# Kernel tuning notes

Hardware: AMD Instinct MI355X
Metric: run time of the kernel (lower is better)

Reference implementation:

```python
import jax, jax.numpy as jnp
import numpy as np

E = 16   # num_experts
K = 4    # num_activated_experts
B, S, H, I = 4, 1024, 1024, 2048


def setup_inputs() -> dict:
    key = jax.random.key(0)
    k0, k1, k2, k3 = jax.random.split(key, 4)
    scale = 0.02
    return {
        "hidden_states": jax.random.normal(k0, (B, S, H), jnp.float32),
        "router_w": jax.random.normal(k1, (H, E), jnp.float32) * scale,
        "router_b": jnp.zeros((E,), jnp.float32),
        "w1": jax.random.normal(k2, (E, H, I), jnp.float32) * scale,
        "b1": jnp.zeros((E, I), jnp.float32),
        "w2": jax.random.normal(k3, (E, I, H), jnp.float32) * scale,
        "b2": jnp.zeros((E, H), jnp.float32),
    }


def reference(hidden_states, router_w, router_b, w1, b1, w2, b2):
    b, s, h = hidden_states.shape
    # router: softmax over experts, pick top-k, renormalize top-k weights
    logits = hidden_states @ router_w + router_b            # [B,S,E]
    probs = jax.nn.softmax(logits, axis=-1)
    topw, topi = jax.lax.top_k(probs, K)                    # [B,S,K]
    topw = topw / jnp.sum(topw, axis=-1, keepdims=True)
    # scatter top-k weights into dense per-expert combine weights [B,S,E]
    combine = jnp.sum(
        jax.nn.one_hot(topi, E, dtype=hidden_states.dtype) * topw[..., None],
        axis=2,
    )
    x = hidden_states.reshape(b * s, h)                     # [T,H]
    c = combine.reshape(b * s, E)                           # [T,E]

    def body(acc, expert):
        w1e, b1e, w2e, b2e, ce = expert
        hmid = jax.nn.gelu(x @ w1e + b1e, approximate=False)  # [T,I]
        return acc + (hmid @ w2e + b2e) * ce[:, None], None

    out, _ = jax.lax.scan(body, jnp.zeros_like(x), (w1, b1, w2, b2, c.T))
    return out.reshape(b, s, h)
```

## Files before the change

### kernel.cpp

```cpp
#include <hip/hip_runtime.h>

#define T_TOK 4096
#define H_DIM 1024
#define I_DIM 2048
#define E_NUM 16
#define K_TOP 4
#define BM 128
#define BK 32
#define MAX_TILES 144
#define PAD_PAIRS (MAX_TILES * BM)
#define RW_Q 4104

typedef __attribute__((ext_vector_type(8))) short s16x8;
typedef __attribute__((ext_vector_type(4))) float f32x4;
typedef __attribute__((ext_vector_type(4))) unsigned short u16x4;
typedef __attribute__((ext_vector_type(8))) unsigned short u16x8;

#define DSR(dst, addr, off) \
  asm volatile("ds_read_b128 %0, %1 offset:" #off : "=v"(dst) : "v"(addr))

__device__ __forceinline__ unsigned short f2bf(float f) {
  unsigned u = __float_as_uint(f);
  u += 0x7fffu + ((u >> 16) & 1u);
  return (unsigned short)(u >> 16);
}

__device__ __forceinline__ void mfma_bf16(const s16x8& a, const s16x8& b, f32x4& c) {
  asm("v_mfma_f32_16x16x32_bf16 %0, %1, %2, %0" : "+v"(c) : "v"(a), "v"(b));
}

__device__ __forceinline__ void gld16(const void* g, void* l) {
  __builtin_amdgcn_global_load_lds(
      (const __attribute__((address_space(1))) unsigned int*)g,
      (__attribute__((address_space(3))) unsigned int*)l, 16, 0, 0);
}

__device__ __forceinline__ int tile_map(const int* counts, int ty, int* tsp) {
  int e = -1, acc = 0, base = 0;
#pragma unroll
  for (int ee = 0; ee < E_NUM; ++ee) {
    int tc = (counts[ee] + 127) >> 7;
    if (ty >= acc && ty < acc + tc) {
      e = ee;
      *tsp = base + ((ty - acc) << 7);
    }
    acc += tc;
    base += tc << 7;
  }
  return e;
}

__global__ __launch_bounds__(256) void router_kernel(
    const float* __restrict__ x, const float* __restrict__ rw,
    const float* __restrict__ rb, int* __restrict__ topi,
    float* __restrict__ topw, int* __restrict__ counts,
    unsigned short* __restrict__ xb) {
  __shared__ float rws[4 * RW_Q];
  const int tid = threadIdx.x;
  {
    const size_t base = (size_t)blockIdx.x * 16 * H_DIM;
#pragma unroll
    for (int it = 0; it < 8; ++it) {
      size_t idx = base + ((size_t)(it * 256 + tid)) * 8;
      f32x4 a = *(const f32x4*)(x + idx);
      f32x4 b = *(const f32x4*)(x + idx + 4);
      u16x8 o;
      o[0] = f2bf(a[0]); o[1] = f2bf(a[1]); o[2] = f2bf(a[2]); o[3] = f2bf(a[3]);
      o[4] = f2bf(b[0]); o[5] = f2bf(b[1]); o[6] = f2bf(b[2]); o[7] = f2bf(b[3]);
      *(u16x8*)(xb + idx) = o;
    }
  }
  for (int idx = tid * 4; idx < H_DIM * E_NUM; idx += 256 * 4) {
    f32x4 v = *(const f32x4*)(rw + idx);
    int h = idx >> 4, e0 = idx & 15;
    *(f32x4*)&rws[(h >> 8) * RW_Q + (h & 255) * 16 + e0] = v;
  }
  __syncthreads();
  const int w = tid >> 6, l = tid & 63;
  const int e = l & 15, q = l >> 4;
  const float rbe = rb[e];
  const float* ldsb = &rws[q * RW_Q + e];
#pragma unroll
  for (int i = 0; i < 4; ++i) {
    const int t = blockIdx.x * 16 + w * 4 + i;
    const float* xr = x + (size_t)t * H_DIM + (q << 8);
    float acc = 0.f;
#pragma unroll 8
    for (int hh = 0; hh < 256; hh += 4) {
      f32x4 xv = *(const f32x4*)(xr + hh);
      acc += xv[0] * ldsb[(hh + 0) * 16];
      acc += xv[1] * ldsb[(hh + 1) * 16];
      acc += xv[2] * ldsb[(hh + 2) * 16];
      acc += xv[3] * ldsb[(hh + 3) * 16];
    }
    acc += __shfl_xor(acc, 16);
    acc += __shfl_xor(acc, 32);
    float logit = acc + rbe;
    float m = logit;
    m = fmaxf(m, __shfl_xor(m, 1));
    m = fmaxf(m, __shfl_xor(m, 2));
    m = fmaxf(m, __shfl_xor(m, 4));
    m = fmaxf(m, __shfl_xor(m, 8));
    float ex = expf(logit - m);
    int rank = 0;
    const int b16 = l & 48;
#pragma unroll
    for (int j = 0; j < 16; ++j) {
      float vj = __shfl(ex, b16 + j);
      rank += (vj > ex) || (vj == ex && j < e);
    }
    float sel = (rank < K_TOP) ? ex : 0.f;
    float subs = sel;
    subs += __shfl_xor(subs, 1);
    subs += __shfl_xor(subs, 2);
    subs += __shfl_xor(subs, 4);
    subs += __shfl_xor(subs, 8);
    if (q == 0 && rank < K_TOP) {
      topi[t * K_TOP + rank] = e;
      topw[t * K_TOP + rank] = ex / subs;
      atomicAdd(&counts[e], 1);
    }
  }
}

__global__ __launch_bounds__(256) void scatter_kernel(
    const int* __restrict__ topi, const float* __restrict__ topw,
    const int* __restrict__ counts, int* __restrict__ cursor,
    int* __restrict__ pairTok, float* __restrict__ pairW,
    int* __restrict__ pairPos) {
  int padBase[E_NUM];
  int base = 0;
#pragma unroll
  for (int ee = 0; ee < E_NUM; ++ee) {
    padBase[ee] = base;
    base += ((counts[ee] + 127) >> 7) << 7;
  }
  const int t = blockIdx.x * 256 + threadIdx.x;
#pragma unroll
  for (int k = 0; k < K_TOP; ++k) {
    int e = topi[t * K_TOP + k];
    int pos = atomicAdd(&cursor[e], 1);
    int idx = padBase[e] + pos;
    pairTok[idx] = t;
    pairW[idx] = topw[t * K_TOP + k];
    pairPos[t * K_TOP + k] = idx;
  }
#pragma unroll
  for (int ee = 0; ee < E_NUM; ++ee) {
    int c = counts[ee];
    int padded = ((c + 127) >> 7) << 7;
    int o = c + t;
    if (o < padded) pairTok[padBase[ee] + o] = -1;
  }
}

__device__ __forceinline__ void transpose_tile(const float* __restrict__ src,
                                               unsigned short* __restrict__ dst,
                                               int R, int C, int tx, int ty) {
  int r0 = ty * 64, c0 = tx * 64;
  __shared__ float tle[64][65];
  int rr = threadIdx.x >> 4, cc = (threadIdx.x & 15) * 4;
#pragma unroll
  for (int i = 0; i < 4; ++i) {
    f32x4 v = *(const f32x4*)(src + (size_t)(r0 + rr + 16 * i) * C + c0 + cc);
    tle[rr + 16 * i][cc + 0] = v[0];
    tle[rr + 16 * i][cc + 1] = v[1];
    tle[rr + 16 * i][cc + 2] = v[2];
    tle[rr + 16 * i][cc + 3] = v[3];
  }
  __syncthreads();
#pragma unroll
  for (int i = 0; i < 4; ++i) {
    int oc = c0 + rr + 16 * i;
    u16x4 o;
    o[0] = f2bf(tle[cc + 0][rr + 16 * i]);
    o[1] = f2bf(tle[cc + 1][rr + 16 * i]);
    o[2] = f2bf(tle[cc + 2][rr + 16 * i]);
    o[3] = f2bf(tle[cc + 3][rr + 16 * i]);
    *(u16x4*)(dst + (size_t)oc * R + r0 + cc) = o;
  }
}

__global__ __launch_bounds__(256) void transpose_kernel(
    const float* __restrict__ src, unsigned short* __restrict__ dst, int R,
    int C) {
  size_t es = (size_t)R * C;
  transpose_tile(src + es * blockIdx.z, dst + es * blockIdx.z, R, C,
                 blockIdx.x, blockIdx.y);
}

__global__ __launch_bounds__(256) void transpose2_kernel(
    const float* __restrict__ w1, const float* __restrict__ w2,
    unsigned short* __restrict__ wT1, unsigned short* __restrict__ wT2) {
  const int bid = blockIdx.x;
  const size_t es = (size_t)H_DIM * I_DIM;
  if (bid < 8192) {
    const int e = bid >> 9, tb = bid & 511;
    transpose_tile(w1 + es * e, wT1 + es * e, H_DIM, I_DIM, tb & 31, tb >> 5);
  } else {
    const int eb = bid - 8192;
    const int e = eb >> 9, tb = eb & 511;
    transpose_tile(w2 + es * e, wT2 + es * e, I_DIM, H_DIM, tb & 15, tb >> 4);
  }
}

__global__ __launch_bounds__(256, 4) void gemm1_kernel(
    const unsigned short* __restrict__ xb, const unsigned short* __restrict__ w1t,
    const float* __restrict__ b1, unsigned short* __restrict__ hmid,
    const int* __restrict__ pairTok, const int* __restrict__ counts) {
  const int bid = blockIdx.x;
  const int lin = (bid & 7) * 288 + (bid >> 3);
  const int tx = lin & 15, ty = lin >> 4;
  int tsp = 0;
  const int e = tile_map(counts, ty, &tsp);
  if (e < 0) return;
  const int n0 = tx * 128;
  __shared__ unsigned short As[2][BM * BK];
  __shared__ unsigned short Bs[2][BM * BK];
  const int tid = threadIdx.x, w = tid >> 6, l = tid & 63;
  const int rbase = w * 16 + (l >> 2);
  const int segp = (l & 3) ^ ((l >> 3) & 3);
  int tok0 = pairTok[tsp + rbase];
  if (tok0 < 0) tok0 = 0;
  int tok1 = pairTok[tsp + rbase + 64];
  if (tok1 < 0) tok1 = 0;
  const char* gA0 = (const char*)(xb + (size_t)tok0 * H_DIM) + segp * 16;
  const char* gA1 = (const char*)(xb + (size_t)tok1 * H_DIM) + segp * 16;
  const unsigned short* wbase = w1t + (size_t)e * I_DIM * H_DIM;
  const char* gB0 = (const char*)(wbase + (size_t)(n0 + rbase) * H_DIM) + segp * 16;
  const char* gB1 = (const char*)(wbase + (size_t)(n0 + rbase + 64) * H_DIM) + segp * 16;

  f32x4 acc[4][4];
#pragma unroll
  for (int m = 0; m < 4; ++m)
#pragma unroll
    for (int n = 0; n < 4; ++n) acc[m][n] = f32x4{0.f, 0.f, 0.f, 0.f};

  const int wr = w >> 1, wc = w & 1, lrow = l & 15, g = l >> 4;
  const int gs = g ^ ((l >> 1) & 3);
  const int NK = H_DIM / BK;

  gld16(gA0, &As[0][w * 512]);
  gld16(gA1, &As[0][2048 + w * 512]);
  gld16(gB0, &Bs[0][w * 512]);
  gld16(gB1, &Bs[0][2048 + w * 512]);

  for (int kt = 0; kt < NK; ++kt) {
    __syncthreads();
    if (kt + 1 < NK) {
      const int kb = (kt + 1) * 64;
      const int nb = (kt + 1) & 1;
      gld16(gA0 + kb, &As[nb][w * 512]);
      gld16(gA1 + kb, &As[nb][2048 + w * 512]);
      gld16(gB0 + kb, &Bs[nb][w * 512]);
      gld16(gB1 + kb, &Bs[nb][2048 + w * 512]);
    }
    const int cb = kt & 1;
    const s16x8* Ap = (const s16x8*)As[cb];
    const s16x8* Bp = (const s16x8*)Bs[cb];
    s16x8 av[4], bv[4];
#pragma unroll
    for (int m = 0; m < 4; ++m) av[m] = Ap[(wr * 64 + m * 16 + lrow) * 4 + gs];
#pragma unroll
    for (int n = 0; n < 4; ++n) bv[n] = Bp[(wc * 64 + n * 16 + lrow) * 4 + gs];
#pragma unroll
    for (int m = 0; m < 4; ++m)
#pragma unroll
      for (int n = 0; n < 4; ++n) mfma_bf16(av[m], bv[n], acc[m][n]);
  }

  const float* b1e = b1 + (size_t)e * I_DIM;
#pragma unroll
  for (int m = 0; m < 4; ++m) {
    const int rw0 = wr * 64 + m * 16 + g * 4;
#pragma unroll
    for (int n = 0; n < 4; ++n) {
      const int col = n0 + wc * 64 + n * 16 + lrow;
      const float bb = b1e[col];
      f32x4 v = acc[m][n];
#pragma unroll
      for (int j = 0; j < 4; ++j) {
        const int p = tsp + rw0 + j;
        float xv = v[j] + bb;
        float y = 0.7978845608028654f * (xv + 0.044715f * xv * xv * xv);
        float ey = __expf(2.f * y);
        float th = 1.f - 2.f / (ey + 1.f);
        float ge = 0.5f * xv * (1.f + th);
        hmid[(size_t)p * I_DIM + col] = f2bf(ge);
      }
    }
  }
}

__global__ __launch_bounds__(256, 3) void gemm2_kernel(
    const unsigned short* __restrict__ hmid,
    const unsigned short* __restrict__ w2t, const float* __restrict__ b2,
    float* __restrict__ out, unsigned short* __restrict__ poA,
    unsigned short* __restrict__ poB, const int* __restrict__ pairTok,
    const float* __restrict__ pairW, const int* __restrict__ counts, int mode) {
  __shared__ char LDS[49152];
  const int bid = blockIdx.x;
  const int nchunk = (mode == 2) ? 288 : 144;
  const int lin = (bid & 7) * nchunk + (bid >> 3);
  const int kh = (mode == 2) ? (lin & 1) : 0;
  const int tx = (mode == 2) ? ((lin >> 1) & 7) : (lin & 7);
  const int ty = (mode == 2) ? (lin >> 4) : (lin >> 3);
  int tsp = 0;
  const int e = tile_map(counts, ty, &tsp);
  if (e < 0) return;
  const int n0 = tx * 128;
  const int tid = threadIdx.x, w = tid >> 6, l = tid & 63;
  const int rbase = w * 16 + (l >> 2);
  const int segp = (l & 3) ^ ((l >> 3) & 3);
  const size_t koff = (size_t)kh * 2048;
  const char* gA0 =
      (const char*)(hmid + (size_t)(tsp + rbase) * I_DIM) + segp * 16 + koff;
  const char* gA1 =
      (const char*)(hmid + (size_t)(tsp + rbase + 64) * I_DIM) + segp * 16 + koff;
  const unsigned short* wbase = w2t + (size_t)e * H_DIM * I_DIM;
  const char* gB0 =
      (const char*)(wbase + (size_t)(n0 + rbase) * I_DIM) + segp * 16 + koff;
  const char* gB1 =
      (const char*)(wbase + (size_t)(n0 + rbase + 64) * I_DIM) + segp * 16 + koff;

  f32x4 acc[4][4];
#pragma unroll
  for (int m = 0; m < 4; ++m)
#pragma unroll
    for (int n = 0; n < 4; ++n) acc[m][n] = f32x4{0.f, 0.f, 0.f, 0.f};

  const int wr = w >> 1, wc = w & 1, lrow = l & 15, g = l >> 4;
  const int gs = g ^ ((l >> 1) & 3);
  const int NK = (mode == 2) ? 32 : 64;

  char* dA = LDS + w * 1024;
  char* dB = LDS + 24576 + w * 1024;
  const unsigned ldsb = (unsigned)(uintptr_t)&LDS[0];
  const unsigned aRd = ldsb + (unsigned)((wr * 64 + lrow) * 64 + gs * 16);
  const unsigned bRd = ldsb + 24576u + (unsigned)((wc * 64 + lrow) * 64 + gs * 16);

  asm volatile("s_waitcnt vmcnt(0)" ::: "memory");
  gld16(gA0, dA);        gld16(gA1, dA + 4096);
  gld16(gB0, dB);        gld16(gB1, dB + 4096);
  gld16(gA0 + 64, dA + 8192);  gld16(gA1 + 64, dA + 8192 + 4096);
  gld16(gB0 + 64, dB + 8192);  gld16(gB1 + 64, dB + 8192 + 4096);

  int srd = 0, sst = 2;
  for (int t = 0; t < NK; ++t) {
    if (t + 1 < NK)
      asm volatile("s_waitcnt vmcnt(4)" ::: "memory");
    else
      asm volatile("s_waitcnt vmcnt(0)" ::: "memory");
    asm volatile("s_barrier" ::: "memory");
    const int tau = t + 2;
    if (tau < NK) {
      const size_t kb = (size_t)tau * 64;
      char* da = dA + sst * 8192;
      char* db = dB + sst * 8192;
      gld16(gA0 + kb, da);  gld16(gA1 + kb, da + 4096);
      gld16(gB0 + kb, db);  gld16(gB1 + kb, db + 4096);
    }
    const unsigned so = (unsigned)(srd * 8192);
    const unsigned aS = aRd + so, bS = bRd + so;
    s16x8 av[4], bv[4];
    DSR(bv[0], bS, 0);    DSR(bv[1], bS, 1024);
    DSR(bv[2], bS, 2048); DSR(bv[3], bS, 3072);
    DSR(av[0], aS, 0);    DSR(av[1], aS, 1024);
    DSR(av[2], aS, 2048); DSR(av[3], aS, 3072);
    asm volatile("s_waitcnt lgkmcnt(0)" ::: "memory");
    __builtin_amdgcn_sched_barrier(0);
    __builtin_amdgcn_s_setprio(1);
#pragma unroll
    for (int m = 0; m < 4; ++m)
#pragma unroll
      for (int n = 0; n < 4; ++n) mfma_bf16(av[m], bv[n], acc[m][n]);
    __builtin_amdgcn_s_setprio(0);
    srd = (srd == 2) ? 0 : srd + 1;
    sst = (sst == 2) ? 0 : sst + 1;
  }
  __builtin_amdgcn_sched_barrier(0);

  if (mode >= 1) {
    unsigned short* po = (kh == 0) ? poA : poB;
#pragma unroll
    for (int m = 0; m < 4; ++m) {
      const int rw0 = wr * 64 + m * 16 + g * 4;
#pragma unroll
      for (int n = 0; n < 4; ++n) {
        const int col = n0 + wc * 64 + n * 16 + lrow;
        f32x4 v = acc[m][n];
#pragma unroll
        for (int j = 0; j < 4; ++j)
          po[(size_t)(tsp + rw0 + j) * H_DIM + col] = f2bf(v[j]);
      }
    }
  } else {
    const float* b2e = b2 + (size_t)e * H_DIM;
#pragma unroll
    for (int m = 0; m < 4; ++m) {
      const int rw0 = wr * 64 + m * 16 + g * 4;
#pragma unroll
      for (int j = 0; j < 4; ++j) {
        const int p = tsp + rw0 + j;
        const int tok = pairTok[p];
        if (tok < 0) continue;
        const float pw = pairW[p];
        float* orow = out + (size_t)tok * H_DIM;
#pragma unroll
        for (int n = 0; n < 4; ++n) {
          const int col = n0 + wc * 64 + n * 16 + lrow;
          float val = (acc[m][n][j] + b2e[col]) * pw;
          atomicAdd(orow + col, val);
        }
      }
    }
  }
}

__global__ __launch_bounds__(256) void combine_kernel(
    const unsigned short* __restrict__ poA, const unsigned short* __restrict__ poB,
    const int* __restrict__ pairPos, const int* __restrict__ topi,
    const float* __restrict__ topw, const float* __restrict__ b2,
    float* __restrict__ out, int nbuf) {
  const int t = blockIdx.x * 2 + (threadIdx.x >> 7);
  const int c0 = (threadIdx.x & 127) * 8;
  float o[8];
#pragma unroll
  for (int j = 0; j < 8; ++j) o[j] = 0.f;
#pragma unroll
  for (int k = 0; k < K_TOP; ++k) {
    const int e = topi[t * K_TOP + k];
    const float pw = topw[t * K_TOP + k];
    const int pos = pairPos[t * K_TOP + k];
    u16x8 va = *(const u16x8*)(poA + (size_t)pos * H_DIM + c0);
    u16x8 vb;
    if (nbuf == 2) vb = *(const u16x8*)(poB + (size_t)pos * H_DIM + c0);
    const float* b2r = b2 + (size_t)e * H_DIM + c0;
#pragma unroll
    for (int j = 0; j < 8; ++j) {
      float hv = __uint_as_float((unsigned)va[j] << 16);
      if (nbuf == 2) hv += __uint_as_float((unsigned)vb[j] << 16);
      o[j] += pw * (hv + b2r[j]);
    }
  }
  float* orow = out + (size_t)t * H_DIM + c0;
  *(f32x4*)orow = f32x4{o[0], o[1], o[2], o[3]};
  *(f32x4*)(orow + 4) = f32x4{o[4], o[5], o[6], o[7]};
}

extern "C" void kernel_launch(void* const* d_in, const int* in_sizes, int n_in,
                              void* d_out, int out_size, void* d_ws,
                              size_t ws_size, hipStream_t stream) {
  const float* x = (const float*)d_in[0];
  const float* rw = (const float*)d_in[1];
  const float* rb = (const float*)d_in[2];
  const float* w1 = (const float*)d_in[3];
  const float* b1 = (const float*)d_in[4];
  const float* w2 = (const float*)d_in[5];
  const float* b2 = (const float*)d_in[6];
  float* out = (float*)d_out;
  char* ws = (char*)d_ws;

  const size_t xbSz = (size_t)T_TOK * H_DIM * 2;
  const size_t poSz = (size_t)PAD_PAIRS * H_DIM * 2;
  const size_t wtSz = (size_t)E_NUM * H_DIM * I_DIM * 2;
  const size_t hmSz = (size_t)PAD_PAIRS * I_DIM * 2;
  const size_t smallSz = (size_t)T_TOK * K_TOP * 4 * 3
                         + (size_t)PAD_PAIRS * 4 * 2 + 128;
  const size_t need3 = poSz * 2 + wtSz * 2 + hmSz + smallSz;
  const size_t need2 = poSz * 2 + wtSz + hmSz + smallSz;
  const size_t need1 = poSz + wtSz + hmSz + smallSz;
  const size_t need0 = xbSz + wtSz + hmSz + smallSz;
  int mode;
  if (ws_size >= need3) mode = 3;
  else if (ws_size >= need2) mode = 2;
  else if (ws_size >= need1) mode = 1;
  else if (ws_size >= need0) mode = 0;
  else return;

  size_t off = 0;
  unsigned short* xb = (unsigned short*)(ws + off);
  unsigned short* poA = (unsigned short*)(ws + off);
  off += (mode >= 1) ? poSz : xbSz;
  unsigned short* poB = (unsigned short*)(ws + off);
  if (mode >= 2) off += poSz;
  unsigned short* wT1 = (unsigned short*)(ws + off);
  off += wtSz;
  unsigned short* wT2 = wT1;
  if (mode == 3) { wT2 = (unsigned short*)(ws + off); off += wtSz; }
  unsigned short* hmid = (unsigned short*)(ws + off);
  off += hmSz;
  int* topi = (int*)(ws + off);      off += (size_t)T_TOK * K_TOP * 4;
  float* topw = (float*)(ws + off);  off += (size_t)T_TOK * K_TOP * 4;
  int* pairPos = (int*)(ws + off);   off += (size_t)T_TOK * K_TOP * 4;
  int* pairTok = (int*)(ws + off);   off += (size_t)PAD_PAIRS * 4;
  float* pairW = (float*)(ws + off); off += (size_t)PAD_PAIRS * 4;
  int* counts = (int*)(ws + off);    off += 64;
  int* cursor = (int*)(ws + off);    off += 64;

  const int gmode = (mode >= 2) ? 2 : mode;

  hipMemsetAsync(counts, 0, 128, stream);
  if (gmode == 0) hipMemsetAsync(out, 0, (size_t)T_TOK * H_DIM * 4, stream);

  router_kernel<<<T_TOK / 16, 256, 0, stream>>>(x, rw, rb, topi, topw, counts,
                                                xb);
  scatter_kernel<<<T_TOK / 256, 256, 0, stream>>>(topi, topw, counts, cursor,
                                                  pairTok, pairW, pairPos);
  if (mode == 3) {
    transpose2_kernel<<<16384, 256, 0, stream>>>(w1, w2, wT1, wT2);
    gemm1_kernel<<<16 * MAX_TILES, 256, 0, stream>>>(xb, wT1, b1, hmid, pairTok,
                                                     counts);
  } else {
    transpose_kernel<<<dim3(I_DIM / 64, H_DIM / 64, E_NUM), 256, 0, stream>>>(
        w1, wT1, H_DIM, I_DIM);
    gemm1_kernel<<<16 * MAX_TILES, 256, 0, stream>>>(xb, wT1, b1, hmid, pairTok,
                                                     counts);
    transpose_kernel<<<dim3(H_DIM / 64, I_DIM / 64, E_NUM), 256, 0, stream>>>(
        w2, wT2, I_DIM, H_DIM);
  }
  gemm2_kernel<<<(gmode == 2 ? 16 : 8) * MAX_TILES, 256, 0, stream>>>(
      hmid, wT2, b2, out, poA, poB, pairTok, pairW, counts, gmode);
  if (gmode >= 1)
    combine_kernel<<<T_TOK / 2, 256, 0, stream>>>(poA, poB, pairPos, topi, topw,
                                                  b2, out, gmode);
}
```

Measured before the change: 412.5 us.

## Fuse router with w1 transpose and overlap w2 transpose with gemm1

```diff
diff --git a/kernel.cpp b/kernel.cpp
--- a/kernel.cpp
+++ b/kernel.cpp
@@ -9,7 +9,6 @@
 #define BK 32
 #define MAX_TILES 144
 #define PAD_PAIRS (MAX_TILES * BM)
-#define RW_Q 4104
 
 typedef __attribute__((ext_vector_type(8))) short s16x8;
 typedef __attribute__((ext_vector_type(4))) float f32x4;
@@ -50,15 +49,41 @@
   return e;
 }
 
-__global__ __launch_bounds__(256) void router_kernel(
-    const float* __restrict__ x, const float* __restrict__ rw,
+__device__ __forceinline__ void transpose_tile(const float* __restrict__ src,
+                                               unsigned short* __restrict__ dst,
+                                               int R, int C, int tx, int ty) {
+  int r0 = ty * 64, c0 = tx * 64;
+  __shared__ float tle[64][65];
+  int rr = threadIdx.x >> 4, cc = (threadIdx.x & 15) * 4;
+#pragma unroll
+  for (int i = 0; i < 4; ++i) {
+    f32x4 v = *(const f32x4*)(src + (size_t)(r0 + rr + 16 * i) * C + c0 + cc);
+    tle[rr + 16 * i][cc + 0] = v[0];
+    tle[rr + 16 * i][cc + 1] = v[1];
+    tle[rr + 16 * i][cc + 2] = v[2];
+    tle[rr + 16 * i][cc + 3] = v[3];
+  }
+  __syncthreads();
+#pragma unroll
+  for (int i = 0; i < 4; ++i) {
+    int oc = c0 + rr + 16 * i;
+    u16x4 o;
+    o[0] = f2bf(tle[cc + 0][rr + 16 * i]);
+    o[1] = f2bf(tle[cc + 1][rr + 16 * i]);
+    o[2] = f2bf(tle[cc + 2][rr + 16 * i]);
+    o[3] = f2bf(tle[cc + 3][rr + 16 * i]);
+    *(u16x4*)(dst + (size_t)oc * R + r0 + cc) = o;
+  }
+}
+
+__device__ __forceinline__ void router_body(
+    int rbid, const float* __restrict__ x, const float* __restrict__ rw,
     const float* __restrict__ rb, int* __restrict__ topi,
     float* __restrict__ topw, int* __restrict__ counts,
     unsigned short* __restrict__ xb) {
-  __shared__ float rws[4 * RW_Q];
   const int tid = threadIdx.x;
   {
-    const size_t base = (size_t)blockIdx.x * 16 * H_DIM;
+    const size_t base = (size_t)rbid * 16 * H_DIM;
 #pragma unroll
     for (int it = 0; it < 8; ++it) {
       size_t idx = base + ((size_t)(it * 256 + tid)) * 8;
@@ -70,28 +95,22 @@
       *(u16x8*)(xb + idx) = o;
     }
   }
-  for (int idx = tid * 4; idx < H_DIM * E_NUM; idx += 256 * 4) {
-    f32x4 v = *(const f32x4*)(rw + idx);
-    int h = idx >> 4, e0 = idx & 15;
-    *(f32x4*)&rws[(h >> 8) * RW_Q + (h & 255) * 16 + e0] = v;
-  }
-  __syncthreads();
   const int w = tid >> 6, l = tid & 63;
   const int e = l & 15, q = l >> 4;
   const float rbe = rb[e];
-  const float* ldsb = &rws[q * RW_Q + e];
+  const float* rq = rw + ((size_t)q * 256) * E_NUM + e;
 #pragma unroll
   for (int i = 0; i < 4; ++i) {
-    const int t = blockIdx.x * 16 + w * 4 + i;
+    const int t = rbid * 16 + w * 4 + i;
     const float* xr = x + (size_t)t * H_DIM + (q << 8);
     float acc = 0.f;
 #pragma unroll 8
     for (int hh = 0; hh < 256; hh += 4) {
       f32x4 xv = *(const f32x4*)(xr + hh);
-      acc += xv[0] * ldsb[(hh + 0) * 16];
-      acc += xv[1] * ldsb[(hh + 1) * 16];
-      acc += xv[2] * ldsb[(hh + 2) * 16];
-      acc += xv[3] * ldsb[(hh + 3) * 16];
+      acc += xv[0] * rq[(hh + 0) * 16];
+      acc += xv[1] * rq[(hh + 1) * 16];
+      acc += xv[2] * rq[(hh + 2) * 16];
+      acc += xv[3] * rq[(hh + 3) * 16];
     }
     acc += __shfl_xor(acc, 16);
     acc += __shfl_xor(acc, 32);
@@ -123,6 +142,30 @@
   }
 }
 
+__global__ __launch_bounds__(256) void fused1_kernel(
+    const float* __restrict__ x, const float* __restrict__ rw,
+    const float* __restrict__ rb, int* __restrict__ topi,
+    float* __restrict__ topw, int* __restrict__ counts,
+    unsigned short* __restrict__ xb, const float* __restrict__ w1,
+    unsigned short* __restrict__ wT1) {
+  const int bid = blockIdx.x;
+  if (bid < 8192) {
+    const size_t es = (size_t)H_DIM * I_DIM;
+    const int e = bid >> 9, tb = bid & 511;
+    transpose_tile(w1 + es * e, wT1 + es * e, H_DIM, I_DIM, tb & 31, tb >> 5);
+  } else {
+    router_body(bid - 8192, x, rw, rb, topi, topw, counts, xb);
+  }
+}
+
+__global__ __launch_bounds__(256) void transpose_kernel(
+    const float* __restrict__ src, unsigned short* __restrict__ dst, int R,
+    int C) {
+  size_t es = (size_t)R * C;
+  transpose_tile(src + es * blockIdx.z, dst + es * blockIdx.z, R, C,
+                 blockIdx.x, blockIdx.y);
+}
+
 __global__ __launch_bounds__(256) void scatter_kernel(
     const int* __restrict__ topi, const float* __restrict__ topw,
     const int* __restrict__ counts, int* __restrict__ cursor,
@@ -154,61 +197,11 @@
   }
 }
 
-__device__ __forceinline__ void transpose_tile(const float* __restrict__ src,
-                                               unsigned short* __restrict__ dst,
-                                               int R, int C, int tx, int ty) {
-  int r0 = ty * 64, c0 = tx * 64;
-  __shared__ float tle[64][65];
-  int rr = threadIdx.x >> 4, cc = (threadIdx.x & 15) * 4;
-#pragma unroll
-  for (int i = 0; i < 4; ++i) {
-    f32x4 v = *(const f32x4*)(src + (size_t)(r0 + rr + 16 * i) * C + c0 + cc);
-    tle[rr + 16 * i][cc + 0] = v[0];
-    tle[rr + 16 * i][cc + 1] = v[1];
-    tle[rr + 16 * i][cc + 2] = v[2];
-    tle[rr + 16 * i][cc + 3] = v[3];
-  }
-  __syncthreads();
-#pragma unroll
-  for (int i = 0; i < 4; ++i) {
-    int oc = c0 + rr + 16 * i;
-    u16x4 o;
-    o[0] = f2bf(tle[cc + 0][rr + 16 * i]);
-    o[1] = f2bf(tle[cc + 1][rr + 16 * i]);
-    o[2] = f2bf(tle[cc + 2][rr + 16 * i]);
-    o[3] = f2bf(tle[cc + 3][rr + 16 * i]);
-    *(u16x4*)(dst + (size_t)oc * R + r0 + cc) = o;
-  }
-}
-
-__global__ __launch_bounds__(256) void transpose_kernel(
-    const float* __restrict__ src, unsigned short* __restrict__ dst, int R,
-    int C) {
-  size_t es = (size_t)R * C;
-  transpose_tile(src + es * blockIdx.z, dst + es * blockIdx.z, R, C,
-                 blockIdx.x, blockIdx.y);
-}
-
-__global__ __launch_bounds__(256) void transpose2_kernel(
-    const float* __restrict__ w1, const float* __restrict__ w2,
-    unsigned short* __restrict__ wT1, unsigned short* __restrict__ wT2) {
-  const int bid = blockIdx.x;
-  const size_t es = (size_t)H_DIM * I_DIM;
-  if (bid < 8192) {
-    const int e = bid >> 9, tb = bid & 511;
-    transpose_tile(w1 + es * e, wT1 + es * e, H_DIM, I_DIM, tb & 31, tb >> 5);
-  } else {
-    const int eb = bid - 8192;
-    const int e = eb >> 9, tb = eb & 511;
-    transpose_tile(w2 + es * e, wT2 + es * e, I_DIM, H_DIM, tb & 15, tb >> 4);
-  }
-}
-
-__global__ __launch_bounds__(256, 4) void gemm1_kernel(
-    const unsigned short* __restrict__ xb, const unsigned short* __restrict__ w1t,
-    const float* __restrict__ b1, unsigned short* __restrict__ hmid,
-    const int* __restrict__ pairTok, const int* __restrict__ counts) {
-  const int bid = blockIdx.x;
+__device__ __forceinline__ void gemm1_body(
+    int bid, const unsigned short* __restrict__ xb,
+    const unsigned short* __restrict__ w1t, const float* __restrict__ b1,
+    unsigned short* __restrict__ hmid, const int* __restrict__ pairTok,
+    const int* __restrict__ counts) {
   const int lin = (bid & 7) * 288 + (bid >> 3);
   const int tx = lin & 15, ty = lin >> 4;
   int tsp = 0;
@@ -289,6 +282,29 @@
         hmid[(size_t)p * I_DIM + col] = f2bf(ge);
       }
     }
+  }
+}
+
+__global__ __launch_bounds__(256, 4) void gemm1_kernel(
+    const unsigned short* __restrict__ xb, const unsigned short* __restrict__ w1t,
+    const float* __restrict__ b1, unsigned short* __restrict__ hmid,
+    const int* __restrict__ pairTok, const int* __restrict__ counts) {
+  gemm1_body(blockIdx.x, xb, w1t, b1, hmid, pairTok, counts);
+}
+
+__global__ __launch_bounds__(256, 3) void fused2_kernel(
+    const unsigned short* __restrict__ xb, const unsigned short* __restrict__ w1t,
+    const float* __restrict__ b1, unsigned short* __restrict__ hmid,
+    const int* __restrict__ pairTok, const int* __restrict__ counts,
+    const float* __restrict__ w2, unsigned short* __restrict__ wT2) {
+  const int bid = blockIdx.x;
+  if (bid < 2304) {
+    gemm1_body(bid, xb, w1t, b1, hmid, pairTok, counts);
+  } else {
+    const int tbid = bid - 2304;
+    const size_t es = (size_t)H_DIM * I_DIM;
+    const int e = tbid >> 9, tb = tbid & 511;
+    transpose_tile(w2 + es * e, wT2 + es * e, I_DIM, H_DIM, tb & 15, tb >> 4);
   }
 }
 
@@ -467,27 +483,28 @@
   const size_t hmSz = (size_t)PAD_PAIRS * I_DIM * 2;
   const size_t smallSz = (size_t)T_TOK * K_TOP * 4 * 3
                          + (size_t)PAD_PAIRS * 4 * 2 + 128;
-  const size_t need3 = poSz * 2 + wtSz * 2 + hmSz + smallSz;
-  const size_t need2 = poSz * 2 + wtSz + hmSz + smallSz;
-  const size_t need1 = poSz + wtSz + hmSz + smallSz;
-  const size_t need0 = xbSz + wtSz + hmSz + smallSz;
-  int mode;
-  if (ws_size >= need3) mode = 3;
-  else if (ws_size >= need2) mode = 2;
-  else if (ws_size >= need1) mode = 1;
-  else if (ws_size >= need0) mode = 0;
-  else return;
+  const size_t needDualSplit = 2 * poSz + 2 * wtSz + hmSz + smallSz;
+  const size_t needDual      = poSz + 2 * wtSz + hmSz + smallSz;
+  const size_t needSplit     = 2 * poSz + wtSz + hmSz + smallSz;
+  const size_t needPo        = poSz + wtSz + hmSz + smallSz;
+  const size_t needMin       = xbSz + wtSz + hmSz + smallSz;
+  int dual = 0, split = 0, po = 0;
+  if (ws_size >= needDualSplit) { dual = 1; split = 1; po = 1; }
+  else if (ws_size >= needDual) { dual = 1; po = 1; }
+  else if (ws_size >= needSplit) { split = 1; po = 1; }
+  else if (ws_size >= needPo) { po = 1; }
+  else if (ws_size < needMin) return;
 
   size_t off = 0;
   unsigned short* xb = (unsigned short*)(ws + off);
   unsigned short* poA = (unsigned short*)(ws + off);
-  off += (mode >= 1) ? poSz : xbSz;
+  off += po ? poSz : xbSz;
   unsigned short* poB = (unsigned short*)(ws + off);
-  if (mode >= 2) off += poSz;
+  if (split) off += poSz;
   unsigned short* wT1 = (unsigned short*)(ws + off);
   off += wtSz;
   unsigned short* wT2 = wT1;
-  if (mode == 3) { wT2 = (unsigned short*)(ws + off); off += wtSz; }
+  if (dual) { wT2 = (unsigned short*)(ws + off); off += wtSz; }
   unsigned short* hmid = (unsigned short*)(ws + off);
   off += hmSz;
   int* topi = (int*)(ws + off);      off += (size_t)T_TOK * K_TOP * 4;
@@ -498,22 +515,19 @@
   int* counts = (int*)(ws + off);    off += 64;
   int* cursor = (int*)(ws + off);    off += 64;
 
-  const int gmode = (mode >= 2) ? 2 : mode;
+  const int gmode = split ? 2 : (po ? 1 : 0);
 
   hipMemsetAsync(counts, 0, 128, stream);
   if (gmode == 0) hipMemsetAsync(out, 0, (size_t)T_TOK * H_DIM * 4, stream);
 
-  router_kernel<<<T_TOK / 16, 256, 0, stream>>>(x, rw, rb, topi, topw, counts,
-                                                xb);
+  fused1_kernel<<<8192 + 256, 256, 0, stream>>>(x, rw, rb, topi, topw, counts,
+                                                xb, w1, wT1);
   scatter_kernel<<<T_TOK / 256, 256, 0, stream>>>(topi, topw, counts, cursor,
                                                   pairTok, pairW, pairPos);
-  if (mode == 3) {
-    transpose2_kernel<<<16384, 256, 0, stream>>>(w1, w2, wT1, wT2);
-    gemm1_kernel<<<16 * MAX_TILES, 256, 0, stream>>>(xb, wT1, b1, hmid, pairTok,
-                                                     counts);
+  if (dual) {
+    fused2_kernel<<<2304 + 8192, 256, 0, stream>>>(xb, wT1, b1, hmid, pairTok,
+                                                   counts, w2, wT2);
   } else {
-    transpose_kernel<<<dim3(I_DIM / 64, H_DIM / 64, E_NUM), 256, 0, stream>>>(
-        w1, wT1, H_DIM, I_DIM);
     gemm1_kernel<<<16 * MAX_TILES, 256, 0, stream>>>(xb, wT1, b1, hmid, pairTok,
                                                      counts);
     transpose_kernel<<<dim3(H_DIM / 64, I_DIM / 64, E_NUM), 256, 0, stream>>>(
```

Result: no change. 412.5 us (-0.0%).
